# Kernel optimization log

Hardware: AMD Instinct MI355X
Metric: run time of the kernel (lower is better)

## Reference

```python
import jax, jax.numpy as jnp
import numpy as np

X_DIM = 512
C_DIM = 512
T = 32768
I_DIM = X_DIM + C_DIM


def setup_inputs() -> dict:
    key = jax.random.key(0)
    ks = jax.random.split(key, 9)
    s = 1.0 / np.sqrt(I_DIM)  # torch nn.Linear default init range
    def lin(kw, kb):
        w = jax.random.uniform(kw, (C_DIM, I_DIM), jnp.float32, -s, s)
        b = jax.random.uniform(kb, (C_DIM,), jnp.float32, -s, s)
        return w, b
    wf_w, wf_b = lin(ks[0], ks[1])
    wi_w, wi_b = lin(ks[2], ks[3])
    wc_w, wc_b = lin(ks[4], ks[5])
    wo_w, wo_b = lin(ks[6], ks[7])
    x_list = jax.random.normal(ks[8], (T, X_DIM), jnp.float32)
    return {"x_list": x_list, "wf_w": wf_w, "wf_b": wf_b, "wi_w": wi_w,
            "wi_b": wi_b, "wc_w": wc_w, "wc_b": wc_b, "wo_w": wo_w, "wo_b": wo_b}


def reference(x_list, wf_w, wf_b, wi_w, wi_b, wc_w, wc_b, wo_w, wo_b):
    c_dim = wf_w.shape[0]
    # Fuse the four gate projections into one GEMV per step (same math:
    # torch Linear y = i @ W.T + b, applied per gate then concatenated).
    W = jnp.concatenate([wf_w, wi_w, wc_w, wo_w], axis=0)  # [4*c_dim, i_dim]
    b = jnp.concatenate([wf_b, wi_b, wc_b, wo_b], axis=0)  # [4*c_dim]

    def step(carry, x):
        c, h = carry
        i = jnp.concatenate([x, h])          # [i_dim]
        g = W @ i + b                         # [4*c_dim]
        ff = jax.nn.sigmoid(g[:c_dim])
        ii = jax.nn.sigmoid(g[c_dim:2 * c_dim])
        cc = jnp.tanh(g[2 * c_dim:3 * c_dim])
        oo = jax.nn.sigmoid(g[3 * c_dim:])
        c = ff * c + ii * cc
        h = jnp.tanh(c) * oo
        return (c, h), None

    init = (jnp.zeros((c_dim,), x_list.dtype), jnp.zeros((c_dim,), x_list.dtype))
    (c, h), _ = jax.lax.scan(step, init, x_list)
    return (c, h)
```

## Files before the change

### kernel.cpp

```cpp
#include <hip/hip_runtime.h>
#include <hip/hip_bf16.h>
#include <cstdint>


#define T_TOTAL 32768
#define NBLK 64

__device__ __forceinline__ float sigm(float x) {
    return 1.0f / (1.0f + __expf(-x));
}
__device__ __forceinline__ float tanh_fast(float x) {
    float ax = fabsf(x);
    float e = __expf(2.0f * ax);
    float t = 1.0f - 2.0f / (e + 1.0f);
    return copysignf(t, x);
}

#define FMA4(a, wv, vv) \
    a = fmaf((wv).x, (vv).x, a); a = fmaf((wv).y, (vv).y, a); \
    a = fmaf((wv).z, (vv).z, a); a = fmaf((wv).w, (vv).w, a)

__global__ __launch_bounds__(256, 1) void lstm_fused(
    const float* __restrict__ x,
    const float* __restrict__ wf, const float* __restrict__ wi,
    const float* __restrict__ wc, const float* __restrict__ wo,
    const float* __restrict__ bf, const float* __restrict__ bi,
    const float* __restrict__ bc, const float* __restrict__ bo,
    unsigned long long* __restrict__ hdq,
    float* __restrict__ out)
{
    __shared__ alignas(16) float4 whlds4[4096];
    __shared__ alignas(16) float4 wxlds4[4096];
    __shared__ alignas(16) float  hl[2][512];

    const int b   = blockIdx.x;
    const int tid = threadIdx.x;
    const int r   = tid >> 5;
    const int seg = tid & 31;
    const int w   = tid >> 6;
    const int l   = tid & 63;

    #pragma unroll
    for (int k = 0; k < 32; ++k) {
        int idx  = k * 256 + tid;
        int sel  = idx >> 12;
        int idx2 = idx & 4095;
        int ll   = idx2 & 63;
        int jj   = (idx2 >> 6) & 3;
        int gg   = (idx2 >> 8) & 3;
        int ww   = idx2 >> 10;
        const float* Wp = (gg == 0) ? wf : (gg == 1) ? wi : (gg == 2) ? wc : wo;
        int row  = b * 8 + ww * 2 + (ll >> 5);
        int col  = 4 * (ll & 31) + 128 * jj + (sel ? 0 : 512);
        float4 v = *(const float4*)(Wp + (size_t)row * 1024 + col);
        if (sel) wxlds4[idx2] = v; else whlds4[idx2] = v;
    }
    const int row = b * 8 + r;
    float4 bias4 = make_float4(bf[row], bi[row], bc[row], bo[row]);

    float cold = 0.f;
    __syncthreads();

    const float4* hl4   = (const float4*)hl;
    const int     wbase = w * 1024 + l;
    const int     lbase = l & 32;

    float a0, a1, a2, a3;
    {
        const float4* xp = (const float4*)x;
        float4 xv0 = xp[seg], xv1 = xp[seg + 32],
               xv2 = xp[seg + 64], xv3 = xp[seg + 96];
        float4 q0, q1, q2, q3;
        a0 = a1 = a2 = a3 = 0.f;
        q0 = wxlds4[wbase +   0]; q1 = wxlds4[wbase +  64];
        q2 = wxlds4[wbase + 128]; q3 = wxlds4[wbase + 192];
        FMA4(a0, q0, xv0); FMA4(a0, q1, xv1); FMA4(a0, q2, xv2); FMA4(a0, q3, xv3);
        q0 = wxlds4[wbase + 256]; q1 = wxlds4[wbase + 320];
        q2 = wxlds4[wbase + 384]; q3 = wxlds4[wbase + 448];
        FMA4(a1, q0, xv0); FMA4(a1, q1, xv1); FMA4(a1, q2, xv2); FMA4(a1, q3, xv3);
        q0 = wxlds4[wbase + 512]; q1 = wxlds4[wbase + 576];
        q2 = wxlds4[wbase + 640]; q3 = wxlds4[wbase + 704];
        FMA4(a2, q0, xv0); FMA4(a2, q1, xv1); FMA4(a2, q2, xv2); FMA4(a2, q3, xv3);
        q0 = wxlds4[wbase + 768]; q1 = wxlds4[wbase + 832];
        q2 = wxlds4[wbase + 896]; q3 = wxlds4[wbase + 960];
        FMA4(a3, q0, xv0); FMA4(a3, q1, xv1); FMA4(a3, q2, xv2); FMA4(a3, q3, xv3);
    }

    for (int s = 0; s < T_TOTAL; ++s) {
        const int sp = (s & 1) ^ 1;
        const int sc = s & 1;

        if (tid < 64) {
            const unsigned need = (unsigned)s;
            const unsigned long long* src =
                hdq + (size_t)sp * 1024 + (tid >> 3) * 16 + (tid & 7);
            unsigned long long v0, v1, v2, v3, v4, v5, v6, v7;
            int guard = 0;
            bool ok = false;
            do {
                v0 = __hip_atomic_load(src,       __ATOMIC_RELAXED, __HIP_MEMORY_SCOPE_AGENT);
                v1 = __hip_atomic_load(src + 128, __ATOMIC_RELAXED, __HIP_MEMORY_SCOPE_AGENT);
                v2 = __hip_atomic_load(src + 256, __ATOMIC_RELAXED, __HIP_MEMORY_SCOPE_AGENT);
                v3 = __hip_atomic_load(src + 384, __ATOMIC_RELAXED, __HIP_MEMORY_SCOPE_AGENT);
                v4 = __hip_atomic_load(src + 512, __ATOMIC_RELAXED, __HIP_MEMORY_SCOPE_AGENT);
                v5 = __hip_atomic_load(src + 640, __ATOMIC_RELAXED, __HIP_MEMORY_SCOPE_AGENT);
                v6 = __hip_atomic_load(src + 768, __ATOMIC_RELAXED, __HIP_MEMORY_SCOPE_AGENT);
                v7 = __hip_atomic_load(src + 896, __ATOMIC_RELAXED, __HIP_MEMORY_SCOPE_AGENT);
                ok = ((unsigned)(v0 >> 32) == need) & ((unsigned)(v1 >> 32) == need)
                   & ((unsigned)(v2 >> 32) == need) & ((unsigned)(v3 >> 32) == need)
                   & ((unsigned)(v4 >> 32) == need) & ((unsigned)(v5 >> 32) == need)
                   & ((unsigned)(v6 >> 32) == need) & ((unsigned)(v7 >> 32) == need);
            } while (!ok && ++guard < (1 << 20));
            hl[sp][tid]       = __uint_as_float((unsigned)v0);
            hl[sp][tid + 64]  = __uint_as_float((unsigned)v1);
            hl[sp][tid + 128] = __uint_as_float((unsigned)v2);
            hl[sp][tid + 192] = __uint_as_float((unsigned)v3);
            hl[sp][tid + 256] = __uint_as_float((unsigned)v4);
            hl[sp][tid + 320] = __uint_as_float((unsigned)v5);
            hl[sp][tid + 384] = __uint_as_float((unsigned)v6);
            hl[sp][tid + 448] = __uint_as_float((unsigned)v7);
        }
        __syncthreads();

        const int snx = (s + 1 < T_TOTAL) ? s + 1 : s;
        const float4* xpn = (const float4*)(x + (size_t)snx * 512);
        float4 nx0 = xpn[seg], nx1 = xpn[seg + 32],
               nx2 = xpn[seg + 64], nx3 = xpn[seg + 96];

        float4 h0 = hl4[sp * 128 + seg];
        float4 h1 = hl4[sp * 128 + seg + 32];
        float4 h2 = hl4[sp * 128 + seg + 64];
        float4 h3 = hl4[sp * 128 + seg + 96];

        float4 w00 = whlds4[wbase +   0], w01 = whlds4[wbase +  64];
        float4 w02 = whlds4[wbase + 128], w03 = whlds4[wbase + 192];
        float4 w10 = whlds4[wbase + 256], w11 = whlds4[wbase + 320];
        float4 w12 = whlds4[wbase + 384], w13 = whlds4[wbase + 448];
        float4 w20 = whlds4[wbase + 512], w21 = whlds4[wbase + 576];
        float4 w22 = whlds4[wbase + 640], w23 = whlds4[wbase + 704];
        float4 w30 = whlds4[wbase + 768], w31 = whlds4[wbase + 832];
        float4 w32 = whlds4[wbase + 896], w33 = whlds4[wbase + 960];

        FMA4(a0, w00, h0); FMA4(a0, w01, h1); FMA4(a0, w02, h2); FMA4(a0, w03, h3);
        FMA4(a1, w10, h0); FMA4(a1, w11, h1); FMA4(a1, w12, h2); FMA4(a1, w13, h3);
        FMA4(a2, w20, h0); FMA4(a2, w21, h1); FMA4(a2, w22, h2); FMA4(a2, w23, h3);
        FMA4(a3, w30, h0); FMA4(a3, w31, h1); FMA4(a3, w32, h2); FMA4(a3, w33, h3);

        #pragma unroll
        for (int m = 1; m < 32; m <<= 1) {
            a0 += __shfl_xor(a0, m);
            a1 += __shfl_xor(a1, m);
            a2 += __shfl_xor(a2, m);
            a3 += __shfl_xor(a3, m);
        }

        float pre = (seg == 1) ? a1 + bias4.y
                  : (seg == 2) ? a2 + bias4.z
                  : (seg == 3) ? a3 + bias4.w
                  :              a0 + bias4.x;
        float act = (seg == 2) ? tanh_fast(pre) : sigm(pre);
        float ff  = __shfl(act, lbase);
        float iiv = __shfl(act, lbase + 1);
        float ccv = __shfl(act, lbase + 2);
        float ov  = __shfl(act, lbase + 3);

        if (seg == 0) {
            cold = fmaf(ff, cold, iiv * ccv);
            float hnew = tanh_fast(cold) * ov;
            unsigned long long tv = ((unsigned long long)(unsigned)(s + 1) << 32)
                                  | (unsigned long long)__float_as_uint(hnew);
            __hip_atomic_store(hdq + (size_t)sc * 1024 + b * 16 + r, tv,
                               __ATOMIC_RELAXED, __HIP_MEMORY_SCOPE_AGENT);
            if (s == T_TOTAL - 1) {
                out[row]       = cold;
                out[512 + row] = hnew;
            }
        }

        float4 q0, q1, q2, q3;
        a0 = a1 = a2 = a3 = 0.f;
        q0 = wxlds4[wbase +   0]; q1 = wxlds4[wbase +  64];
        q2 = wxlds4[wbase + 128]; q3 = wxlds4[wbase + 192];
        FMA4(a0, q0, nx0); FMA4(a0, q1, nx1); FMA4(a0, q2, nx2); FMA4(a0, q3, nx3);
        q0 = wxlds4[wbase + 256]; q1 = wxlds4[wbase + 320];
        q2 = wxlds4[wbase + 384]; q3 = wxlds4[wbase + 448];
        FMA4(a1, q0, nx0); FMA4(a1, q1, nx1); FMA4(a1, q2, nx2); FMA4(a1, q3, nx3);
        q0 = wxlds4[wbase + 512]; q1 = wxlds4[wbase + 576];
        q2 = wxlds4[wbase + 640]; q3 = wxlds4[wbase + 704];
        FMA4(a2, q0, nx0); FMA4(a2, q1, nx1); FMA4(a2, q2, nx2); FMA4(a2, q3, nx3);
        q0 = wxlds4[wbase + 768]; q1 = wxlds4[wbase + 832];
        q2 = wxlds4[wbase + 896]; q3 = wxlds4[wbase + 960];
        FMA4(a3, q0, nx0); FMA4(a3, q1, nx1); FMA4(a3, q2, nx2); FMA4(a3, q3, nx3);
    }
}

extern "C" void kernel_launch(void* const* d_in, const int* in_sizes, int n_in,
                              void* d_out, int out_size, void* d_ws, size_t ws_size,
                              hipStream_t stream)
{
    const float* x  = (const float*)d_in[0];
    const float* wf = (const float*)d_in[1];
    const float* bf = (const float*)d_in[2];
    const float* wi = (const float*)d_in[3];
    const float* bi = (const float*)d_in[4];
    const float* wc = (const float*)d_in[5];
    const float* bc = (const float*)d_in[6];
    const float* wo = (const float*)d_in[7];
    const float* bo = (const float*)d_in[8];
    float* out = (float*)d_out;

    unsigned long long* hdq = (unsigned long long*)d_ws;

    hipMemsetAsync(d_ws, 0, 16384, stream);

    lstm_fused<<<NBLK, 256, 0, stream>>>(x, wf, wi, wc, wo,
                                         bf, bi, bc, bo, hdq, out);
}
```

Baseline: 56.36 ms.

## Have every thread poll its own h values directly, dropping LDS staging and barrier

Each thread now spin-loads, straight from the global handoff queue, the 16 tagged h entries it needs, waiting until all lanes in its wave see the current step tag. This replaces the scheme where 64 threads polled, staged h into shared memory, and the whole block waited at a __syncthreads. The aim is to cut the per-step barrier and LDS round trip on the serial critical path. In exchange, all 256 threads issue 16 atomic loads each per poll, which raises L2 polling traffic, and a timeout now exits the loop instead of continuing.

Result: slower. 117.3 ms (+108.0%).

```diff
diff --git a/kernel.cpp b/kernel.cpp
--- a/kernel.cpp
+++ b/kernel.cpp
@@ -31,7 +31,6 @@
 {
     __shared__ alignas(16) float4 whlds4[4096];
     __shared__ alignas(16) float4 wxlds4[4096];
-    __shared__ alignas(16) float  hl[2][512];
 
     const int b   = blockIdx.x;
     const int tid = threadIdx.x;
@@ -61,9 +60,9 @@
     float cold = 0.f;
     __syncthreads();
 
-    const float4* hl4   = (const float4*)hl;
-    const int     wbase = w * 1024 + l;
-    const int     lbase = l & 32;
+    const int wbase = w * 1024 + l;
+    const int lbase = l & 32;
+    const int pbase = ((seg >> 1) << 4) + ((seg & 1) << 2);
 
     float a0, a1, a2, a3;
     {
@@ -90,47 +89,56 @@
         const int sp = (s & 1) ^ 1;
         const int sc = s & 1;
 
-        if (tid < 64) {
-            const unsigned need = (unsigned)s;
-            const unsigned long long* src =
-                hdq + (size_t)sp * 1024 + (tid >> 3) * 16 + (tid & 7);
-            unsigned long long v0, v1, v2, v3, v4, v5, v6, v7;
+        const unsigned need = (unsigned)s;
+        const unsigned long long* base = hdq + (size_t)sp * 1024 + pbase;
+        unsigned long long v00, v01, v02, v03, v10, v11, v12, v13;
+        unsigned long long v20, v21, v22, v23, v30, v31, v32, v33;
+        bool dead = false;
+        {
             int guard = 0;
-            bool ok = false;
+            bool ok;
             do {
-                v0 = __hip_atomic_load(src,       __ATOMIC_RELAXED, __HIP_MEMORY_SCOPE_AGENT);
-                v1 = __hip_atomic_load(src + 128, __ATOMIC_RELAXED, __HIP_MEMORY_SCOPE_AGENT);
-                v2 = __hip_atomic_load(src + 256, __ATOMIC_RELAXED, __HIP_MEMORY_SCOPE_AGENT);
-                v3 = __hip_atomic_load(src + 384, __ATOMIC_RELAXED, __HIP_MEMORY_SCOPE_AGENT);
-                v4 = __hip_atomic_load(src + 512, __ATOMIC_RELAXED, __HIP_MEMORY_SCOPE_AGENT);
-                v5 = __hip_atomic_load(src + 640, __ATOMIC_RELAXED, __HIP_MEMORY_SCOPE_AGENT);
-                v6 = __hip_atomic_load(src + 768, __ATOMIC_RELAXED, __HIP_MEMORY_SCOPE_AGENT);
-                v7 = __hip_atomic_load(src + 896, __ATOMIC_RELAXED, __HIP_MEMORY_SCOPE_AGENT);
-                ok = ((unsigned)(v0 >> 32) == need) & ((unsigned)(v1 >> 32) == need)
-                   & ((unsigned)(v2 >> 32) == need) & ((unsigned)(v3 >> 32) == need)
-                   & ((unsigned)(v4 >> 32) == need) & ((unsigned)(v5 >> 32) == need)
-                   & ((unsigned)(v6 >> 32) == need) & ((unsigned)(v7 >> 32) == need);
-            } while (!ok && ++guard < (1 << 20));
-            hl[sp][tid]       = __uint_as_float((unsigned)v0);
-            hl[sp][tid + 64]  = __uint_as_float((unsigned)v1);
-            hl[sp][tid + 128] = __uint_as_float((unsigned)v2);
-            hl[sp][tid + 192] = __uint_as_float((unsigned)v3);
-            hl[sp][tid + 256] = __uint_as_float((unsigned)v4);
-            hl[sp][tid + 320] = __uint_as_float((unsigned)v5);
-            hl[sp][tid + 384] = __uint_as_float((unsigned)v6);
-            hl[sp][tid + 448] = __uint_as_float((unsigned)v7);
+#define PLD(X, off) X = __hip_atomic_load(base + (off), __ATOMIC_RELAXED, \
+                                          __HIP_MEMORY_SCOPE_AGENT)
+                PLD(v00,   0); PLD(v01,   1); PLD(v02,   2); PLD(v03,   3);
+                PLD(v10, 256); PLD(v11, 257); PLD(v12, 258); PLD(v13, 259);
+                PLD(v20, 512); PLD(v21, 513); PLD(v22, 514); PLD(v23, 515);
+                PLD(v30, 768); PLD(v31, 769); PLD(v32, 770); PLD(v33, 771);
+#undef PLD
+                ok = ((unsigned)(v00 >> 32) == need) & ((unsigned)(v01 >> 32) == need)
+                   & ((unsigned)(v02 >> 32) == need) & ((unsigned)(v03 >> 32) == need)
+                   & ((unsigned)(v10 >> 32) == need) & ((unsigned)(v11 >> 32) == need)
+                   & ((unsigned)(v12 >> 32) == need) & ((unsigned)(v13 >> 32) == need)
+                   & ((unsigned)(v20 >> 32) == need) & ((unsigned)(v21 >> 32) == need)
+                   & ((unsigned)(v22 >> 32) == need) & ((unsigned)(v23 >> 32) == need)
+                   & ((unsigned)(v30 >> 32) == need) & ((unsigned)(v31 >> 32) == need)
+                   & ((unsigned)(v32 >> 32) == need) & ((unsigned)(v33 >> 32) == need);
+                if (++guard >= (1 << 17)) { dead = true; break; }
+            } while (!__all(ok));
         }
-        __syncthreads();
+        if (__any(dead)) break;
+
+        float4 h0 = make_float4(__uint_as_float((unsigned)v00),
+                                __uint_as_float((unsigned)v01),
+                                __uint_as_float((unsigned)v02),
+                                __uint_as_float((unsigned)v03));
+        float4 h1 = make_float4(__uint_as_float((unsigned)v10),
+                                __uint_as_float((unsigned)v11),
+                                __uint_as_float((unsigned)v12),
+                                __uint_as_float((unsigned)v13));
+        float4 h2 = make_float4(__uint_as_float((unsigned)v20),
+                                __uint_as_float((unsigned)v21),
+                                __uint_as_float((unsigned)v22),
+                                __uint_as_float((unsigned)v23));
+        float4 h3 = make_float4(__uint_as_float((unsigned)v30),
+                                __uint_as_float((unsigned)v31),
+                                __uint_as_float((unsigned)v32),
+                                __uint_as_float((unsigned)v33));
 
         const int snx = (s + 1 < T_TOTAL) ? s + 1 : s;
         const float4* xpn = (const float4*)(x + (size_t)snx * 512);
         float4 nx0 = xpn[seg], nx1 = xpn[seg + 32],
                nx2 = xpn[seg + 64], nx3 = xpn[seg + 96];
-
-        float4 h0 = hl4[sp * 128 + seg];
-        float4 h1 = hl4[sp * 128 + seg + 32];
-        float4 h2 = hl4[sp * 128 + seg + 64];
-        float4 h3 = hl4[sp * 128 + seg + 96];
 
         float4 w00 = whlds4[wbase +   0], w01 = whlds4[wbase +  64];
         float4 w02 = whlds4[wbase + 128], w03 = whlds4[wbase + 192];
```
